# Optimization experiments

Hardware: AMD Instinct MI355X
Metric: run time of the kernel (lower is better)

The kernel has to match this reference:

```python
import jax, jax.numpy as jnp
import numpy as np

B, DIN, DP, DOUT, K, N = 4, 64, 3, 64, 16, 8192


def setup_inputs() -> dict:
    key = jax.random.key(0)
    ks = jax.random.split(key, 5)
    features = jax.random.normal(ks[0], (B, DIN, N), dtype=jnp.float32)
    positions = jax.random.normal(ks[1], (B, DP, N), dtype=jnp.float32)
    neighborhoods = jax.random.randint(ks[2], (B, K, N), 0, N, dtype=jnp.int32)
    position_theta = jax.random.normal(ks[3], (DP, DIN, DOUT), dtype=jnp.float32) * 0.05
    position_bias = jnp.zeros((DIN, DOUT), dtype=jnp.float32)
    feature_bias = jnp.zeros((DOUT, 1), dtype=jnp.float32)
    return {
        "features": features,
        "positions": positions,
        "neighborhoods": neighborhoods,
        "position_theta": position_theta,
        "position_bias": position_bias,
        "feature_bias": feature_bias,
    }


def _gather_neighbors(x, idx):
    # x: [D, N], idx: [K, N] -> [D, K, N]
    return x[:, idx]


def reference(features, positions, neighborhoods, position_theta, position_bias, feature_bias):
    # Gather neighbor features/positions: [B, D, K, N]
    fg = jax.vmap(_gather_neighbors)(features, neighborhoods)      # [B, Din, K, N]
    pg = jax.vmap(_gather_neighbors)(positions, neighborhoods)     # [B, Dp,  K, N]
    # Relative positions of neighbors w.r.t. center point
    rel = pg - positions[:, :, None, :]                            # [B, Dp, K, N]
    # Dynamic weight w[b,k,n] = theta . rel + bias, contracted with
    # gathered features and summed over K, without materializing [Din,Dout] per neighbor.
    y = jnp.einsum('pio,bpkn,bikn->bon', position_theta, rel, fg)
    y = y + jnp.einsum('io,bikn->bon', position_bias, fg)
    # feature bias [Dout, 1] broadcasts over [B, Dout, N]
    y = y + feature_bias[None, :, :]
    return y  # [B, Dout, N]; activation=None (linear)
```

## Files before the change

kernel.cpp:

```cpp
#include <hip/hip_runtime.h>

#define NB    4
#define DIN_  64
#define DOUT_ 64
#define KN    16
#define NPT   8192
#define CPAD  264

typedef __attribute__((ext_vector_type(8))) short short8;
typedef __attribute__((ext_vector_type(4))) float v4f;

__device__ __forceinline__ float bf2f(unsigned short u) {
    unsigned int x = ((unsigned int)u) << 16;
    float f; __builtin_memcpy(&f, &x, 4); return f;
}
__device__ __forceinline__ unsigned short f2bf(float f) {
    unsigned int x; __builtin_memcpy(&x, &f, 4);
    x += 0x7fffu + ((x >> 16) & 1u);
    return (unsigned short)(x >> 16);
}

__global__ void k_prep(const float* __restrict__ feat, const float* __restrict__ pos,
                       const float* __restrict__ theta, const float* __restrict__ pbias,
                       unsigned short* __restrict__ ft, float4* __restrict__ pt,
                       unsigned short* __restrict__ tbf) {
    __shared__ float tile[64][65];
    const int bid = blockIdx.x;
    if (bid < 512) {
        int b = bid >> 7, n0 = (bid & 127) << 6;
        int lane = threadIdx.x & 63, w = threadIdx.x >> 6;
#pragma unroll
        for (int r = 0; r < 16; ++r) {
            int i = (r << 2) | w;
            tile[i][lane] = feat[(b*DIN_ + i)*NPT + n0 + lane];
        }
        __syncthreads();
#pragma unroll
        for (int r = 0; r < 16; ++r) {
            int n = (r << 2) | w;
            ft[((size_t)(b*NPT + n0 + n))*DIN_ + lane] = f2bf(tile[lane][n]);
        }
    } else if (bid < 640) {
        int t = (bid - 512)*256 + threadIdx.x;
        int b = t >> 13, n = t & 8191;
        float4 v;
        v.x = pos[(b*3 + 0)*NPT + n];
        v.y = pos[(b*3 + 1)*NPT + n];
        v.z = pos[(b*3 + 2)*NPT + n];
        v.w = 1.0f;
        pt[t] = v;
    } else {
        int e = (bid - 640)*256 + threadIdx.x;
        int o = e >> 5, g = e & 31;
        short8 u;
#pragma unroll
        for (int j = 0; j < 8; ++j) {
            int c = g*8 + j;
            float v = (c < 192) ? theta[c*64 + o] : pbias[(c - 192)*64 + o];
            u[j] = (short)f2bf(v);
        }
        *reinterpret_cast<short8*>(tbf + o*256 + g*8) = u;
    }
}

template<bool USE_WS>
__global__ __launch_bounds__(256, 4) void k_main(
    const float*          __restrict__ feat,
    const float*          __restrict__ pos,
    const int*            __restrict__ nbr,
    const float*          __restrict__ theta,
    const float*          __restrict__ pbias,
    const float*          __restrict__ fbias,
    const unsigned short* __restrict__ ft,
    const float4*         __restrict__ pt,
    const unsigned short* __restrict__ tbf,
    float*                __restrict__ out)
{
    __shared__ __align__(16) unsigned short Xt[32*CPAD];
    __shared__ int    nbs[KN*32];
    __shared__ float4 pcs[32];

    const int tid  = threadIdx.x;
    const int lane = tid & 63;
    const int w    = tid >> 6;
    const int j16  = lane & 15;
    const int pt2  = lane >> 4;

    const int base = blockIdx.x << 5;
    const int b    = base >> 13;
    const int nb0  = base & 8191;

#pragma unroll
    for (int r = 0; r < 2; ++r) {
        int idx = tid + (r << 8);
        int k = idx >> 5, c = idx & 31;
        nbs[idx] = nbr[(b*KN + k)*NPT + nb0 + c];
    }
    if (tid < 128) {
        if (USE_WS) {
            ((float*)pcs)[tid] = ((const float*)(pt + b*NPT + nb0))[tid];
        } else if (tid < 32) {
            int n = nb0 + tid;
            pcs[tid] = make_float4(pos[(b*3+0)*NPT + n], pos[(b*3+1)*NPT + n],
                                   pos[(b*3+2)*NPT + n], 1.0f);
        }
    }
    __syncthreads();

    const unsigned short* ftb = ft + (((size_t)b) << 19);

#pragma unroll
    for (int pass = 0; pass < 2; ++pass) {
        const int q = (w << 3) + (pass << 2) + pt2;
        const float4 pc = pcs[q];
        float acc[4][4];
#pragma unroll
        for (int p = 0; p < 4; ++p)
#pragma unroll
            for (int j = 0; j < 4; ++j) acc[p][j] = 0.f;

#pragma unroll 4
        for (int k = 0; k < KN; ++k) {
            const int id = nbs[(k << 5) + q];
            float4 pg; float f[4];
            if (USE_WS) {
                pg = pt[b*NPT + id];
                ushort4 fr = *reinterpret_cast<const ushort4*>(
                    ftb + (((size_t)id) << 6) + (j16 << 2));
                f[0]=bf2f(fr.x); f[1]=bf2f(fr.y); f[2]=bf2f(fr.z); f[3]=bf2f(fr.w);
            } else {
                pg.x = pos[(b*3+0)*NPT + id];
                pg.y = pos[(b*3+1)*NPT + id];
                pg.z = pos[(b*3+2)*NPT + id];
                pg.w = 1.0f;
#pragma unroll
                for (int j = 0; j < 4; ++j)
                    f[j] = feat[(b*DIN_ + (j16<<2) + j)*NPT + id];
            }
#pragma unroll
            for (int j = 0; j < 4; ++j) {
                acc[0][j] += pg.x * f[j];
                acc[1][j] += pg.y * f[j];
                acc[2][j] += pg.z * f[j];
                acc[3][j] += f[j];
            }
        }
#pragma unroll
        for (int j = 0; j < 4; ++j) {
            acc[0][j] -= pc.x * acc[3][j];
            acc[1][j] -= pc.y * acc[3][j];
            acc[2][j] -= pc.z * acc[3][j];
        }
#pragma unroll
        for (int p = 0; p < 4; ++p) {
            ushort4 pk;
            pk.x = f2bf(acc[p][0]); pk.y = f2bf(acc[p][1]);
            pk.z = f2bf(acc[p][2]); pk.w = f2bf(acc[p][3]);
            *reinterpret_cast<ushort4*>(&Xt[q*CPAD + (p<<6) + (j16<<2)]) = pk;
        }
    }
    __syncthreads();

    const int kg   = pt2;
    const int orow = (w << 4) + j16;
    v4f acc0 = {0.f,0.f,0.f,0.f}, acc1 = {0.f,0.f,0.f,0.f};
#pragma unroll
    for (int ks = 0; ks < 8; ++ks) {
        const int koff = (ks << 5) + (kg << 3);
        short8 a;
        if (USE_WS) {
            a = *reinterpret_cast<const short8*>(tbf + orow*256 + koff);
        } else {
#pragma unroll
            for (int j = 0; j < 8; ++j) {
                int c = koff + j;
                float v = (c < 192) ? theta[c*64 + orow] : pbias[(c - 192)*64 + orow];
                a[j] = (short)f2bf(v);
            }
        }
        short8 b0 = *reinterpret_cast<const short8*>(&Xt[j16*CPAD + koff]);
        short8 b1 = *reinterpret_cast<const short8*>(&Xt[(16 + j16)*CPAD + koff]);
        acc0 = __builtin_amdgcn_mfma_f32_16x16x32_bf16(a, b0, acc0, 0, 0, 0);
        acc1 = __builtin_amdgcn_mfma_f32_16x16x32_bf16(a, b1, acc1, 0, 0, 0);
    }
#pragma unroll
    for (int r = 0; r < 4; ++r) {
        const int o = (w << 4) + (kg << 2) + r;
        const float fb = fbias[o];
        const size_t rowoff = (size_t)(b*DOUT_ + o)*NPT + nb0;
        out[rowoff + j16]      = acc0[r] + fb;
        out[rowoff + 16 + j16] = acc1[r] + fb;
    }
}

extern "C" void kernel_launch(void* const* d_in, const int* in_sizes, int n_in,
                              void* d_out, int out_size, void* d_ws, size_t ws_size,
                              hipStream_t stream) {
    const float* feat  = (const float*)d_in[0];
    const float* pos   = (const float*)d_in[1];
    const int*   nbr   = (const int*)d_in[2];
    const float* theta = (const float*)d_in[3];
    const float* pbias = (const float*)d_in[4];
    const float* fbias = (const float*)d_in[5];
    float* out = (float*)d_out;

    const size_t ft_bytes  = (size_t)NB*NPT*DIN_*2;
    const size_t pt_bytes  = (size_t)NB*NPT*sizeof(float4);
    const size_t tbf_bytes = (size_t)DOUT_*256*2;
    const int n_blocks = (NB*NPT)/32;

    if (ws_size >= ft_bytes + pt_bytes + tbf_bytes) {
        unsigned short* ft  = (unsigned short*)d_ws;
        float4*         pt  = (float4*)((char*)d_ws + ft_bytes);
        unsigned short* tbf = (unsigned short*)((char*)d_ws + ft_bytes + pt_bytes);
        k_prep<<<648, 256, 0, stream>>>(feat, pos, theta, pbias, ft, pt, tbf);
        k_main<true><<<n_blocks, 256, 0, stream>>>(feat, pos, nbr, theta, pbias, fbias,
                                                   ft, pt, tbf, out);
    } else {
        k_main<false><<<n_blocks, 256, 0, stream>>>(feat, pos, nbr, theta, pbias, fbias,
                                                    (const unsigned short*)feat,
                                                    (const float4*)feat,
                                                    (const unsigned short*)feat, out);
    }
}
```

Before: 89.44 us.

## Fuse prep and main kernels into one cooperative launch with grid sync

Merges the layout-conversion prep work (bf16 transpose of features, packed positions, bf16 theta) into the main kernel, placing it in the first blocks of a cooperative launch. A grid-wide barrier separates the prep stage from the gather/MFMA stage, removing one kernel launch and the gap between the two kernels. The transpose tile reuses the Xt shared buffer. This depends on all 1024 blocks being co-resident, which is checked through an occupancy query with a fallback path. In exchange it adds the cost of a grid-wide barrier and any cooperative-launch overhead.

```diff
diff --git a/kernel.cpp b/kernel.cpp
--- a/kernel.cpp
+++ b/kernel.cpp
@@ -1,4 +1,7 @@
 #include <hip/hip_runtime.h>
+#include <hip/hip_cooperative_groups.h>
+
+namespace cg = cooperative_groups;
 
 #define NB    4
 #define DIN_  64
@@ -63,19 +66,21 @@
     }
 }
 
-template<bool USE_WS>
-__global__ __launch_bounds__(256, 4) void k_main(
-    const float*          __restrict__ feat,
-    const float*          __restrict__ pos,
-    const int*            __restrict__ nbr,
-    const float*          __restrict__ theta,
-    const float*          __restrict__ pbias,
-    const float*          __restrict__ fbias,
-    const unsigned short* __restrict__ ft,
-    const float4*         __restrict__ pt,
-    const unsigned short* __restrict__ tbf,
-    float*                __restrict__ out)
+template<int MODE>
+__global__ __launch_bounds__(256, 4) void k_fused(
+    const float*    __restrict__ feat,
+    const float*    __restrict__ pos,
+    const int*      __restrict__ nbr,
+    const float*    __restrict__ theta,
+    const float*    __restrict__ pbias,
+    const float*    __restrict__ fbias,
+    unsigned short* __restrict__ ft,
+    float4*         __restrict__ pt,
+    unsigned short* __restrict__ tbf,
+    float*          __restrict__ out)
 {
+    constexpr bool USE_WS = (MODE != 2);
+
     __shared__ __align__(16) unsigned short Xt[32*CPAD];
     __shared__ int    nbs[KN*32];
     __shared__ float4 pcs[32];
@@ -85,8 +90,48 @@
     const int w    = tid >> 6;
     const int j16  = lane & 15;
     const int pt2  = lane >> 4;
-
-    const int base = blockIdx.x << 5;
+    const int bid  = blockIdx.x;
+
+    if constexpr (MODE == 1) {
+        if (bid < 512) {
+            float (*tile)[65] = reinterpret_cast<float(*)[65]>(Xt);
+            int b = bid >> 7, n0 = (bid & 127) << 6;
+#pragma unroll
+            for (int r = 0; r < 16; ++r) {
+                int i = (r << 2) | w;
+                tile[i][lane] = feat[(b*DIN_ + i)*NPT + n0 + lane];
+            }
+            __syncthreads();
+#pragma unroll
+            for (int r = 0; r < 16; ++r) {
+                int n = (r << 2) | w;
+                ft[((size_t)(b*NPT + n0 + n))*DIN_ + lane] = f2bf(tile[lane][n]);
+            }
+        } else if (bid < 640) {
+            int t = (bid - 512)*256 + tid;
+            int b = t >> 13, n = t & 8191;
+            float4 v;
+            v.x = pos[(b*3 + 0)*NPT + n];
+            v.y = pos[(b*3 + 1)*NPT + n];
+            v.z = pos[(b*3 + 2)*NPT + n];
+            v.w = 1.0f;
+            pt[t] = v;
+        } else if (bid < 648) {
+            int e = (bid - 640)*256 + tid;
+            int o = e >> 5, g = e & 31;
+            short8 u;
+#pragma unroll
+            for (int j = 0; j < 8; ++j) {
+                int c = g*8 + j;
+                float v = (c < 192) ? theta[c*64 + o] : pbias[(c - 192)*64 + o];
+                u[j] = (short)f2bf(v);
+            }
+            *reinterpret_cast<short8*>(tbf + o*256 + g*8) = u;
+        }
+        cg::this_grid().sync();
+    }
+
+    const int base = bid << 5;
     const int b    = base >> 13;
     const int nb0  = base & 8191;
 
@@ -213,13 +258,29 @@
         unsigned short* ft  = (unsigned short*)d_ws;
         float4*         pt  = (float4*)((char*)d_ws + ft_bytes);
         unsigned short* tbf = (unsigned short*)((char*)d_ws + ft_bytes + pt_bytes);
-        k_prep<<<648, 256, 0, stream>>>(feat, pos, theta, pbias, ft, pt, tbf);
-        k_main<true><<<n_blocks, 256, 0, stream>>>(feat, pos, nbr, theta, pbias, fbias,
-                                                   ft, pt, tbf, out);
+
+        static int coop = -1;
+        if (coop < 0) {
+            int nb = 0;
+            hipError_t e = hipOccupancyMaxActiveBlocksPerMultiprocessor(
+                &nb, reinterpret_cast<const void*>(&k_fused<1>), 256, 0);
+            coop = (e == hipSuccess && nb >= 4) ? 1 : 0;
+        }
+
+        if (coop) {
+            void* args[] = { (void*)&feat, (void*)&pos, (void*)&nbr, (void*)&theta,
+                             (void*)&pbias, (void*)&fbias, (void*)&ft, (void*)&pt,
+                             (void*)&tbf, (void*)&out };
+            hipLaunchCooperativeKernel(reinterpret_cast<void*>(&k_fused<1>),
+                                       dim3(n_blocks), dim3(256), args, 0, stream);
+        } else {
+            k_prep<<<648, 256, 0, stream>>>(feat, pos, theta, pbias, ft, pt, tbf);
+            k_fused<0><<<n_blocks, 256, 0, stream>>>(feat, pos, nbr, theta, pbias, fbias,
+                                                     ft, pt, tbf, out);
+        }
     } else {
-        k_main<false><<<n_blocks, 256, 0, stream>>>(feat, pos, nbr, theta, pbias, fbias,
-                                                    (const unsigned short*)feat,
-                                                    (const float4*)feat,
-                                                    (const unsigned short*)feat, out);
-    }
-}
+        k_fused<2><<<n_blocks, 256, 0, stream>>>(feat, pos, nbr, theta, pbias, fbias,
+                                                 (unsigned short*)d_out, (float4*)d_out,
+                                                 (unsigned short*)d_out, out);
+    }
+}
```

After: 89.62 us. No clear change (+0.2%).

## Double-buffer neighbor gathers into LDS via async global_load_lds

Applied to the files above, without the earlier changes.

Splits the workspace path into its own kernel, which gathers neighbor feature rows and positions with global_load_lds into double-buffered shared-memory stages. Each stage covers two neighbors, and the gather for the next stage is issued before the current one is consumed, using explicit vmcnt waits and barriers. The goal is to overlap gather latency with the accumulation math instead of stalling on scattered per-thread global loads. In exchange it adds about 18KB of LDS per block, which may reduce occupancy, and adds two block barriers per stage.

```diff
diff --git a/kernel.cpp b/kernel.cpp
--- a/kernel.cpp
+++ b/kernel.cpp
@@ -9,6 +9,8 @@
 
 typedef __attribute__((ext_vector_type(8))) short short8;
 typedef __attribute__((ext_vector_type(4))) float v4f;
+typedef const __attribute__((address_space(1))) unsigned int as1_u32;
+typedef __attribute__((address_space(3))) unsigned int as3_u32;
 
 __device__ __forceinline__ float bf2f(unsigned short u) {
     unsigned int x = ((unsigned int)u) << 16;
@@ -63,13 +65,8 @@
     }
 }
 
-template<bool USE_WS>
-__global__ __launch_bounds__(256, 4) void k_main(
-    const float*          __restrict__ feat,
-    const float*          __restrict__ pos,
+__global__ __launch_bounds__(256, 4) void k_main_ws(
     const int*            __restrict__ nbr,
-    const float*          __restrict__ theta,
-    const float*          __restrict__ pbias,
     const float*          __restrict__ fbias,
     const unsigned short* __restrict__ ft,
     const float4*         __restrict__ pt,
@@ -77,6 +74,8 @@
     float*                __restrict__ out)
 {
     __shared__ __align__(16) unsigned short Xt[32*CPAD];
+    __shared__ __align__(16) unsigned short stg[2][64*64];
+    __shared__ __align__(16) float4 ptS[2][64];
     __shared__ int    nbs[KN*32];
     __shared__ float4 pcs[32];
 
@@ -96,18 +95,155 @@
         int k = idx >> 5, c = idx & 31;
         nbs[idx] = nbr[(b*KN + k)*NPT + nb0 + c];
     }
-    if (tid < 128) {
-        if (USE_WS) {
-            ((float*)pcs)[tid] = ((const float*)(pt + b*NPT + nb0))[tid];
-        } else if (tid < 32) {
-            int n = nb0 + tid;
-            pcs[tid] = make_float4(pos[(b*3+0)*NPT + n], pos[(b*3+1)*NPT + n],
-                                   pos[(b*3+2)*NPT + n], 1.0f);
-        }
-    }
+    if (tid < 128)
+        ((float*)pcs)[tid] = ((const float*)(pt + b*NPT + nb0))[tid];
     __syncthreads();
 
     const unsigned short* ftb = ft + (((size_t)b) << 19);
+    const float4*         ptb = pt + b*NPT;
+
+    const int qq = lane >> 3;
+    const int fo = (lane & 7) << 3;
+
+    auto ISSUE = [&](int c, int bi) {
+#pragma unroll
+        for (int j = 0; j < 2; ++j) {
+            int s  = (w << 4) + (j << 3) + qq;
+            int kk = s >> 5, q = s & 31;
+            int id = nbs[(((c << 1) + kk) << 5) + q];
+            const unsigned short* gp = ftb + (((size_t)id) << 6) + fo;
+            __builtin_amdgcn_global_load_lds(
+                (as1_u32*)gp,
+                (as3_u32*)&stg[bi][((w << 4) + (j << 3)) << 6],
+                16, 0, 0);
+        }
+        if (lane < 16) {
+            int s  = (w << 4) + lane;
+            int kk = s >> 5, q = s & 31;
+            int id = nbs[(((c << 1) + kk) << 5) + q];
+            __builtin_amdgcn_global_load_lds(
+                (as1_u32*)(ptb + id),
+                (as3_u32*)&ptS[bi][w << 4],
+                16, 0, 0);
+        }
+    };
+
+    float acc[2][4][4];
+#pragma unroll
+    for (int ps = 0; ps < 2; ++ps)
+#pragma unroll
+        for (int p = 0; p < 4; ++p)
+#pragma unroll
+            for (int j = 0; j < 4; ++j) acc[ps][p][j] = 0.f;
+
+    ISSUE(0, 0);
+#pragma unroll
+    for (int c = 0; c < 8; ++c) {
+        __builtin_amdgcn_sched_barrier(0);
+        if (c < 7) ISSUE(c + 1, (c + 1) & 1);
+        __builtin_amdgcn_sched_barrier(0);
+        if (c < 7) asm volatile("s_waitcnt vmcnt(3)" ::: "memory");
+        else       asm volatile("s_waitcnt vmcnt(0)" ::: "memory");
+        __builtin_amdgcn_sched_barrier(0);
+        __builtin_amdgcn_s_barrier();
+
+        const int bi = c & 1;
+#pragma unroll
+        for (int ps = 0; ps < 2; ++ps) {
+            const int q = (w << 3) + (ps << 2) + pt2;
+#pragma unroll
+            for (int kk = 0; kk < 2; ++kk) {
+                const int s = (kk << 5) + q;
+                const float4 pg = ptS[bi][s];
+                ushort4 fr = *reinterpret_cast<const ushort4*>(
+                    &stg[bi][(s << 6) + (j16 << 2)]);
+                float f[4] = { bf2f(fr.x), bf2f(fr.y), bf2f(fr.z), bf2f(fr.w) };
+#pragma unroll
+                for (int j = 0; j < 4; ++j) {
+                    acc[ps][0][j] += pg.x * f[j];
+                    acc[ps][1][j] += pg.y * f[j];
+                    acc[ps][2][j] += pg.z * f[j];
+                    acc[ps][3][j] += f[j];
+                }
+            }
+        }
+        __builtin_amdgcn_s_barrier();
+    }
+
+#pragma unroll
+    for (int ps = 0; ps < 2; ++ps) {
+        const int q = (w << 3) + (ps << 2) + pt2;
+        const float4 pc = pcs[q];
+#pragma unroll
+        for (int j = 0; j < 4; ++j) {
+            acc[ps][0][j] -= pc.x * acc[ps][3][j];
+            acc[ps][1][j] -= pc.y * acc[ps][3][j];
+            acc[ps][2][j] -= pc.z * acc[ps][3][j];
+        }
+#pragma unroll
+        for (int p = 0; p < 4; ++p) {
+            ushort4 pk;
+            pk.x = f2bf(acc[ps][p][0]); pk.y = f2bf(acc[ps][p][1]);
+            pk.z = f2bf(acc[ps][p][2]); pk.w = f2bf(acc[ps][p][3]);
+            *reinterpret_cast<ushort4*>(&Xt[q*CPAD + (p<<6) + (j16<<2)]) = pk;
+        }
+    }
+    __syncthreads();
+
+    const int kg   = pt2;
+    const int orow = (w << 4) + j16;
+    v4f acc0 = {0.f,0.f,0.f,0.f}, acc1 = {0.f,0.f,0.f,0.f};
+#pragma unroll
+    for (int ks = 0; ks < 8; ++ks) {
+        const int koff = (ks << 5) + (kg << 3);
+        short8 a  = *reinterpret_cast<const short8*>(tbf + orow*256 + koff);
+        short8 b0 = *reinterpret_cast<const short8*>(&Xt[j16*CPAD + koff]);
+        short8 b1 = *reinterpret_cast<const short8*>(&Xt[(16 + j16)*CPAD + koff]);
+        acc0 = __builtin_amdgcn_mfma_f32_16x16x32_bf16(a, b0, acc0, 0, 0, 0);
+        acc1 = __builtin_amdgcn_mfma_f32_16x16x32_bf16(a, b1, acc1, 0, 0, 0);
+    }
+#pragma unroll
+    for (int r = 0; r < 4; ++r) {
+        const int o = (w << 4) + (kg << 2) + r;
+        const float fb = fbias[o];
+        const size_t rowoff = (size_t)(b*DOUT_ + o)*NPT + nb0;
+        out[rowoff + j16]      = acc0[r] + fb;
+        out[rowoff + 16 + j16] = acc1[r] + fb;
+    }
+}
+
+__global__ __launch_bounds__(256, 4) void k_main_f(
+    const float* __restrict__ feat, const float* __restrict__ pos,
+    const int*   __restrict__ nbr,  const float* __restrict__ theta,
+    const float* __restrict__ pbias, const float* __restrict__ fbias,
+    float*       __restrict__ out)
+{
+    __shared__ __align__(16) unsigned short Xt[32*CPAD];
+    __shared__ int    nbs[KN*32];
+    __shared__ float4 pcs[32];
+
+    const int tid  = threadIdx.x;
+    const int lane = tid & 63;
+    const int w    = tid >> 6;
+    const int j16  = lane & 15;
+    const int pt2  = lane >> 4;
+
+    const int base = blockIdx.x << 5;
+    const int b    = base >> 13;
+    const int nb0  = base & 8191;
+
+#pragma unroll
+    for (int r = 0; r < 2; ++r) {
+        int idx = tid + (r << 8);
+        int k = idx >> 5, c = idx & 31;
+        nbs[idx] = nbr[(b*KN + k)*NPT + nb0 + c];
+    }
+    if (tid < 32) {
+        int n = nb0 + tid;
+        pcs[tid] = make_float4(pos[(b*3+0)*NPT + n], pos[(b*3+1)*NPT + n],
+                               pos[(b*3+2)*NPT + n], 1.0f);
+    }
+    __syncthreads();
 
 #pragma unroll
     for (int pass = 0; pass < 2; ++pass) {
@@ -123,20 +259,13 @@
         for (int k = 0; k < KN; ++k) {
             const int id = nbs[(k << 5) + q];
             float4 pg; float f[4];
-            if (USE_WS) {
-                pg = pt[b*NPT + id];
-                ushort4 fr = *reinterpret_cast<const ushort4*>(
-                    ftb + (((size_t)id) << 6) + (j16 << 2));
-                f[0]=bf2f(fr.x); f[1]=bf2f(fr.y); f[2]=bf2f(fr.z); f[3]=bf2f(fr.w);
-            } else {
-                pg.x = pos[(b*3+0)*NPT + id];
-                pg.y = pos[(b*3+1)*NPT + id];
-                pg.z = pos[(b*3+2)*NPT + id];
-                pg.w = 1.0f;
-#pragma unroll
-                for (int j = 0; j < 4; ++j)
-                    f[j] = feat[(b*DIN_ + (j16<<2) + j)*NPT + id];
-            }
+            pg.x = pos[(b*3+0)*NPT + id];
+            pg.y = pos[(b*3+1)*NPT + id];
+            pg.z = pos[(b*3+2)*NPT + id];
+            pg.w = 1.0f;
+#pragma unroll
+            for (int j = 0; j < 4; ++j)
+                f[j] = feat[(b*DIN_ + (j16<<2) + j)*NPT + id];
 #pragma unroll
             for (int j = 0; j < 4; ++j) {
                 acc[0][j] += pg.x * f[j];
@@ -168,15 +297,11 @@
     for (int ks = 0; ks < 8; ++ks) {
         const int koff = (ks << 5) + (kg << 3);
         short8 a;
-        if (USE_WS) {
-            a = *reinterpret_cast<const short8*>(tbf + orow*256 + koff);
-        } else {
-#pragma unroll
-            for (int j = 0; j < 8; ++j) {
-                int c = koff + j;
-                float v = (c < 192) ? theta[c*64 + orow] : pbias[(c - 192)*64 + orow];
-                a[j] = (short)f2bf(v);
-            }
+#pragma unroll
+        for (int j = 0; j < 8; ++j) {
+            int c = koff + j;
+            float v = (c < 192) ? theta[c*64 + orow] : pbias[(c - 192)*64 + orow];
+            a[j] = (short)f2bf(v);
         }
         short8 b0 = *reinterpret_cast<const short8*>(&Xt[j16*CPAD + koff]);
         short8 b1 = *reinterpret_cast<const short8*>(&Xt[(16 + j16)*CPAD + koff]);
@@ -214,12 +339,8 @@
         float4*         pt  = (float4*)((char*)d_ws + ft_bytes);
         unsigned short* tbf = (unsigned short*)((char*)d_ws + ft_bytes + pt_bytes);
         k_prep<<<648, 256, 0, stream>>>(feat, pos, theta, pbias, ft, pt, tbf);
-        k_main<true><<<n_blocks, 256, 0, stream>>>(feat, pos, nbr, theta, pbias, fbias,
-                                                   ft, pt, tbf, out);
+        k_main_ws<<<n_blocks, 256, 0, stream>>>(nbr, fbias, ft, pt, tbf, out);
     } else {
-        k_main<false><<<n_blocks, 256, 0, stream>>>(feat, pos, nbr, theta, pbias, fbias,
-                                                    (const unsigned short*)feat,
-                                                    (const float4*)feat,
-                                                    (const unsigned short*)feat, out);
-    }
-}
+        k_main_f<<<n_blocks, 256, 0, stream>>>(feat, pos, nbr, theta, pbias, fbias, out);
+    }
+}
```

Result: slower. 128.1 us (+43.2%).
